# Performance work log

Measured on AMD Instinct MI355X. Metric: run time of the kernel, lower is better.

## Reference

```python
import jax, jax.numpy as jnp
import numpy as np

M, LAM, MAX_ITER, TOL, BETA = 5, 1e-4, 50, 0.01, 1.0


def anderson_fixed_point(lin_w, lin_b, x0):
    """Anderson acceleration for x = Linear(x), faithful to the torch loop.
    x0: (bsz, d, H, W); the fixed-point map applies the linear over W."""
    bsz = x0.shape[0]
    n = x0.size // bsz
    shape = x0.shape
    dt = x0.dtype

    def f(v_flat):  # (bsz, n) -> (bsz, n)
        return (v_flat.reshape(shape) @ lin_w.T + lin_b).reshape(bsz, n)

    x0f = x0.reshape(bsz, n)
    F0 = f(x0f)
    X = jnp.zeros((bsz, M, n), dt).at[:, 0].set(x0f).at[:, 1].set(F0)
    Fm = jnp.zeros((bsz, M, n), dt).at[:, 0].set(F0).at[:, 1].set(f(F0))
    y = jnp.zeros((bsz, M + 1), dt).at[:, 0].set(1.0)
    eyeM = jnp.eye(M, dtype=dt)

    def cond(c):
        _, _, k, res = c
        return (k < MAX_ITER) & (res >= TOL)

    def body(c):
        X, Fm, k, _ = c
        nk = jnp.minimum(k, M)
        # mask inactive history slots (k < M early iterations); padded rows/cols
        # get lam on the diagonal and 0 border -> alpha_j = 0 there, identical
        # to torch's solve on the leading (n+1)x(n+1) submatrix.
        mask = (jnp.arange(M) < nk).astype(dt)               # (M,)
        G = (Fm - X) * mask[None, :, None]                   # (bsz, M, n)
        Hin = jnp.einsum('bin,bjn->bij', G, G) + LAM * eyeM  # (bsz, M, M)
        H = jnp.zeros((bsz, M + 1, M + 1), dt)
        H = H.at[:, 0, 1:].set(mask).at[:, 1:, 0].set(mask).at[:, 1:, 1:].set(Hin)
        alpha = jnp.linalg.solve(H, y[..., None])[:, 1:, 0]  # (bsz, M)
        xnew = BETA * jnp.einsum('bm,bmn->bn', alpha, Fm) + (1.0 - BETA) * jnp.einsum('bm,bmn->bn', alpha, X)
        idx = k % M
        X = X.at[:, idx].set(xnew)
        fnew = f(xnew)
        Fm = Fm.at[:, idx].set(fnew)
        res = jnp.linalg.norm(fnew - xnew) / (1e-5 + jnp.linalg.norm(fnew))
        return (X, Fm, k + 1, res)

    Xf, _, kf, _ = jax.lax.while_loop(
        cond, body, (X, Fm, jnp.int32(2), jnp.asarray(jnp.inf, dt)))
    return Xf[:, (kf - 1) % M].reshape(shape)


def setup_inputs() -> dict:
    key = jax.random.key(0)
    k1, k2, k3, k4, k5 = jax.random.split(key, 5)
    B, D, H, W = 16, 8, 128, 512  # in_features = out_features = W = 512
    x = jax.random.normal(k1, (B, D, H, W), jnp.float32)
    # contractive inner linear so the fixed-point iteration behaves
    lin_w = jax.random.normal(k2, (W, W), jnp.float32) * 0.02
    lin_b = jax.random.normal(k3, (W,), jnp.float32) * 0.1
    weight = jax.random.normal(k4, (W, W), jnp.float32) * 0.02
    bias = jax.random.normal(k5, (W,), jnp.float32) * 0.1
    return {"x": x, "lin_w": lin_w, "lin_b": lin_b, "weight": weight, "bias": bias}


def reference(x, lin_w, lin_b, weight, bias):
    # torch runs the solver under no_grad -> stop_gradient for fidelity
    x_star = anderson_fixed_point(
        jax.lax.stop_gradient(lin_w),
        jax.lax.stop_gradient(lin_b),
        jax.lax.stop_gradient(x))
    return x_star @ weight.T + bias
```

## Files before the change

### kernel.cpp

```cpp
#include <hip/hip_runtime.h>
#include <math.h>

#define FD     512
#define NBATCH 16
#define NROWS  16384
#define ROWS   64
#define NBLK   (NROWS/ROWS)
#define TPB    1024
#define MM     5
#define LAMV   1e-4f
#define MAXIT  50
#define TOLV   0.01f
#define NTOT   8388608
#define PADW   520

typedef __attribute__((ext_vector_type(8))) short  short8;
typedef __attribute__((ext_vector_type(4))) float  float4v;

__device__ unsigned short g_Fm[MM][NTOT];
__device__ unsigned short g_G [MM][NTOT];
__device__ unsigned short g_xb[NTOT];
__device__ unsigned short g_Wb [FD*FD];
__device__ unsigned short g_WbO[FD*FD];
__device__ float g_acc [MAXIT-2][NBATCH][8];
__device__ float g_acc0[NBATCH][8];

static __device__ __forceinline__ unsigned short f2bf(float f) {
    unsigned u = __float_as_uint(f);
    u += 0x7fff + ((u >> 16) & 1);
    return (unsigned short)(u >> 16);
}
static __device__ __forceinline__ float bf2f(unsigned short s) {
    return __uint_as_float(((unsigned)s) << 16);
}

template<int MODE>
static __device__ __forceinline__ void mfma_gemm(const unsigned short* __restrict__ Wb,
                                                 const float* __restrict__ bvec,
                                                 const unsigned short* AsIn,
                                                 unsigned short* FsOut,
                                                 float* __restrict__ gout)
{
    const int lane = threadIdx.x & 63;
    const int wv   = threadIdx.x >> 6;
    const int lm   = lane & 15;
    const int quad = lane >> 4;
    float4v acc[4][2];
#pragma unroll
    for (int ct = 0; ct < 2; ct++) {
        const float b = bvec[wv*32 + ct*16 + lm];
#pragma unroll
        for (int r16 = 0; r16 < 4; r16++) {
            acc[r16][ct][0]=b; acc[r16][ct][1]=b; acc[r16][ct][2]=b; acc[r16][ct][3]=b;
        }
    }
#pragma unroll
    for (int q = 0; q < 4; q++) {
#pragma unroll
        for (int kb = 0; kb < 4; kb++) {
            const int ko = q*128 + kb*32 + quad*8;
            short8 bf[2];
#pragma unroll
            for (int ct = 0; ct < 2; ct++)
                bf[ct] = *(const short8*)(Wb + (wv*32 + ct*16 + lm)*FD + ko);
            short8 af[4];
#pragma unroll
            for (int r16 = 0; r16 < 4; r16++)
                af[r16] = *(const short8*)(AsIn + (r16*16 + lm)*PADW + ko);
#pragma unroll
            for (int r16 = 0; r16 < 4; r16++) {
                acc[r16][0] = __builtin_amdgcn_mfma_f32_16x16x32_bf16(af[r16], bf[0], acc[r16][0], 0,0,0);
                acc[r16][1] = __builtin_amdgcn_mfma_f32_16x16x32_bf16(af[r16], bf[1], acc[r16][1], 0,0,0);
            }
        }
    }
#pragma unroll
    for (int ct = 0; ct < 2; ct++) {
        const int c = wv*32 + ct*16 + lm;
#pragma unroll
        for (int r16 = 0; r16 < 4; r16++)
#pragma unroll
            for (int r = 0; r < 4; r++) {
                const int row = r16*16 + quad*4 + r;
                if (MODE == 0) FsOut[row*PADW + c] = f2bf(acc[r16][ct][r]);
                else           gout[row*FD + c]    = acc[r16][ct][r];
            }
    }
}

static __device__ __forceinline__ void red6(const float vals[6], float (*redS)[8], float* accrow)
{
    const int lane = threadIdx.x & 63, wv = threadIdx.x >> 6;
#pragma unroll
    for (int j = 0; j < 6; j++) {
        float v = vals[j];
#pragma unroll
        for (int o = 32; o; o >>= 1) v += __shfl_down(v, o);
        if (lane == 0) redS[wv][j] = v;
    }
    __syncthreads();
    if (threadIdx.x < 6) {
        float s = 0.f;
#pragma unroll
        for (int w = 0; w < 16; w++) s += redS[w][threadIdx.x];
        atomicAdd(accrow + threadIdx.x, s);
    }
}

__global__ void __launch_bounds__(256) k_init0(const float* __restrict__ lin_w,
                                               const float* __restrict__ weight)
{
    const int i0 = blockIdx.x*256 + threadIdx.x, stride = gridDim.x*256;
    for (int i = i0; i < FD*FD; i += stride) {
        g_Wb [i] = f2bf(lin_w[i]);
        g_WbO[i] = f2bf(weight[i]);
    }
    float* a = &g_acc[0][0][0];
    for (int i = i0; i < (MAXIT-2)*NBATCH*8; i += stride) a[i] = 0.f;
    float* a0 = &g_acc0[0][0];
    for (int i = i0; i < NBATCH*8; i += stride) a0[i] = 0.f;
}

__global__ void __launch_bounds__(TPB, 4) k_init1(const float* __restrict__ x,
                                                  const float* __restrict__ lin_b)
{
    __shared__ __align__(16) unsigned short As[ROWS*PADW];
    __shared__ __align__(16) unsigned short Fs[ROWS*PADW];
    __shared__ float redS[16][8];
    const int tid = threadIdx.x;
    const int t = blockIdx.x, b = t >> 4;
    const int base = t * (ROWS*FD);

#pragma unroll
    for (int i = 0; i < 4; i++) {
        const int e = (i*TPB + tid) * 8;
        const float4 a0 = *(const float4*)(x + base + e);
        const float4 a1 = *(const float4*)(x + base + e + 4);
        short8 v;
        v[0]=f2bf(a0.x); v[1]=f2bf(a0.y); v[2]=f2bf(a0.z); v[3]=f2bf(a0.w);
        v[4]=f2bf(a1.x); v[5]=f2bf(a1.y); v[6]=f2bf(a1.z); v[7]=f2bf(a1.w);
        *(short8*)(As + (e>>9)*PADW + (e&511)) = v;
    }
    __syncthreads();
    mfma_gemm<0>(g_Wb, lin_b, As, Fs, nullptr);
    __syncthreads();
    float d00 = 0.f;
#pragma unroll
    for (int i = 0; i < 4; i++) {
        const int e = (i*TPB + tid) * 8;
        const int off = base + e, lo = (e>>9)*PADW + (e&511);
        const short8 fv = *(const short8*)(Fs + lo);
        const short8 xv = *(const short8*)(As + lo);
        short8 gv;
#pragma unroll
        for (int j = 0; j < 8; j++) {
            const float g = bf2f((unsigned short)fv[j]) - bf2f((unsigned short)xv[j]);
            gv[j] = (short)f2bf(g);
            d00 = fmaf(g, g, d00);
        }
        *(short8*)(&g_Fm[0][off]) = fv;
        *(short8*)(&g_G [0][off]) = gv;
    }
    __syncthreads();
    mfma_gemm<0>(g_Wb, lin_b, Fs, As, nullptr);
    __syncthreads();
    float d01 = 0.f, d11 = 0.f;
#pragma unroll
    for (int i = 0; i < 4; i++) {
        const int e = (i*TPB + tid) * 8;
        const int off = base + e, lo = (e>>9)*PADW + (e&511);
        const short8 f1 = *(const short8*)(As + lo);
        const short8 f0 = *(const short8*)(Fs + lo);
        const short8 g0 = *(const short8*)(&g_G[0][off]);
        short8 gv;
#pragma unroll
        for (int j = 0; j < 8; j++) {
            const float g = bf2f((unsigned short)f1[j]) - bf2f((unsigned short)f0[j]);
            gv[j] = (short)f2bf(g);
            d11 = fmaf(g, g, d11);
            d01 = fmaf(bf2f((unsigned short)g0[j]), g, d01);
        }
        *(short8*)(&g_Fm[1][off]) = f1;
        *(short8*)(&g_G [1][off]) = gv;
    }
    const float vals[6] = {d00, d01, d11, 0.f, 0.f, 0.f};
    red6(vals, redS, &g_acc0[b][0]);
}

__global__ void __launch_bounds__(TPB, 4) k_iter(const float* __restrict__ lin_b, int k)
{
    __shared__ __align__(16) unsigned short As[ROWS*PADW];
    __shared__ __align__(16) unsigned short Fs[ROWS*PADW];
    __shared__ float gramS[MM][MM];
    __shared__ float alphaS[MM];
    __shared__ float Hs[48];
    __shared__ float redS[16][8];
    __shared__ float sres;

    const int tid = threadIdx.x;
    const int t = blockIdx.x, b = t >> 4;
    const int base = t * (ROWS*FD);
    const int it = k - 2, idx = k % MM, nk = (k < MM) ? k : MM;

    if (k > 2) {
        float v = 0.f;
        if (tid < 32) {
            const int bb = tid & 15;
            const int jj = (tid < 16) ? ((k-1) % MM) : 5;
            v = g_acc[it-1][bb][jj];
        }
        v += __shfl_xor(v, 1); v += __shfl_xor(v, 2);
        v += __shfl_xor(v, 4); v += __shfl_xor(v, 8);
        const float num = __shfl(v, 0), den = __shfl(v, 16);
        if (tid == 0) sres = sqrtf(num) / (1e-5f + sqrtf(den));
    }
    __syncthreads();
    if (k > 2 && sres < TOLV) return;

    if (tid == 0) {
#pragma unroll
        for (int i = 0; i < MM; i++)
#pragma unroll
            for (int j = 0; j < MM; j++) gramS[i][j] = 0.f;
        gramS[0][0] = g_acc0[b][0];
        gramS[0][1] = gramS[1][0] = g_acc0[b][1];
        gramS[1][1] = g_acc0[b][2];
        const int j0 = (k - 5 > 2) ? (k - 5) : 2;
        for (int j = j0; j < k; j++) {
            const int ij = j % MM, nkj = (j < MM) ? j : MM;
            for (int c = 0; c < MM; c++)
                if (c < nkj || c == ij) {
                    const float vv = g_acc[j-2][b][c];
                    gramS[ij][c] = vv; gramS[c][ij] = vv;
                }
        }
        float* H = Hs;
        for (int i = 0; i < 42; i++) H[i] = 0.f;
        for (int j = 0; j < nk; j++) { H[1+j] = 1.f; H[(1+j)*7] = 1.f; }
#pragma unroll
        for (int i = 0; i < MM; i++) H[(1+i)*7 + (1+i)] = LAMV;
        for (int i = 0; i < nk; i++)
            for (int j = 0; j < nk; j++)
                H[(1+i)*7 + (1+j)] = gramS[i][j] + (i == j ? LAMV : 0.f);
        H[6] = 1.f;
        for (int col = 0; col < 6; col++) {
            int p = col; float mx = fabsf(H[col*7+col]);
            for (int r2 = col+1; r2 < 6; r2++) {
                const float vv = fabsf(H[r2*7+col]);
                if (vv > mx) { mx = vv; p = r2; }
            }
            if (p != col)
                for (int j = col; j < 7; j++) { const float tt = H[col*7+j]; H[col*7+j] = H[p*7+j]; H[p*7+j] = tt; }
            const float piv = H[col*7+col];
            for (int r2 = col+1; r2 < 6; r2++) {
                const float fct = H[r2*7+col] / piv;
                for (int j = col+1; j < 7; j++) H[r2*7+j] -= fct * H[col*7+j];
            }
        }
        for (int r2 = 5; r2 >= 0; r2--) {
            float s = H[r2*7+6];
            for (int j = r2+1; j < 6; j++) s -= H[r2*7+j] * H[j*7+6];
            H[r2*7+6] = s / H[r2*7+r2];
        }
#pragma unroll
        for (int m = 0; m < MM; m++) alphaS[m] = H[(1+m)*7+6];
    }
    __syncthreads();

    float al[MM];
#pragma unroll
    for (int m = 0; m < MM; m++) al[m] = alphaS[m];

    if (nk == MM) {
#pragma unroll
        for (int i = 0; i < 4; i++) {
            const int e = (i*TPB + tid) * 8;
            const int off = base + e;
            float s[8] = {0,0,0,0,0,0,0,0};
#pragma unroll
            for (int m = 0; m < MM; m++) {
                const short8 fm = *(const short8*)(&g_Fm[m][off]);
#pragma unroll
                for (int j = 0; j < 8; j++)
                    s[j] = fmaf(al[m], bf2f((unsigned short)fm[j]), s[j]);
            }
            short8 v;
#pragma unroll
            for (int j = 0; j < 8; j++) v[j] = (short)f2bf(s[j]);
            *(short8*)(As + (e>>9)*PADW + (e&511)) = v;
            *(short8*)(&g_xb[off]) = v;
        }
    } else {
#pragma unroll
        for (int i = 0; i < 4; i++) {
            const int e = (i*TPB + tid) * 8;
            const int off = base + e;
            float s[8] = {0,0,0,0,0,0,0,0};
            for (int m = 0; m < nk; m++) {
                const short8 fm = *(const short8*)(&g_Fm[m][off]);
#pragma unroll
                for (int j = 0; j < 8; j++)
                    s[j] = fmaf(al[m], bf2f((unsigned short)fm[j]), s[j]);
            }
            short8 v;
#pragma unroll
            for (int j = 0; j < 8; j++) v[j] = (short)f2bf(s[j]);
            *(short8*)(As + (e>>9)*PADW + (e&511)) = v;
            *(short8*)(&g_xb[off]) = v;
        }
    }
    __syncthreads();
    mfma_gemm<0>(g_Wb, lin_b, As, Fs, nullptr);
    __syncthreads();
    float dv[6] = {0,0,0,0,0,0};
    float dself = 0.f;
#pragma unroll
    for (int i = 0; i < 4; i++) {
        const int e = (i*TPB + tid) * 8;
        const int off = base + e, lo = (e>>9)*PADW + (e&511);
        const short8 fv = *(const short8*)(Fs + lo);
        const short8 xv = *(const short8*)(As + lo);
        float gg[8]; short8 gv;
#pragma unroll
        for (int j = 0; j < 8; j++) {
            const float ff = bf2f((unsigned short)fv[j]);
            const float g  = ff - bf2f((unsigned short)xv[j]);
            gg[j] = g; gv[j] = (short)f2bf(g);
            dv[5] = fmaf(ff, ff, dv[5]);
            dself = fmaf(g, g, dself);
        }
        *(short8*)(&g_Fm[idx][off]) = fv;
        *(short8*)(&g_G [idx][off]) = gv;
#pragma unroll
        for (int js = 0; js < MM; js++) {
            if (js != idx && js < nk) {
                const short8 gj = *(const short8*)(&g_G[js][off]);
#pragma unroll
                for (int j = 0; j < 8; j++)
                    dv[js] = fmaf(gg[j], bf2f((unsigned short)gj[j]), dv[js]);
            }
        }
    }
    float vals[6];
#pragma unroll
    for (int j = 0; j < MM; j++) vals[j] = (j == idx) ? (dv[j] + dself) : dv[j];
    vals[5] = dv[5];
    red6(vals, redS, &g_acc[it][b][0]);
}

__global__ void __launch_bounds__(TPB, 4) k_final(const float* __restrict__ bias,
                                                  float* __restrict__ out)
{
    __shared__ __align__(16) unsigned short As[ROWS*PADW];
    const int tid = threadIdx.x;
    const int base = blockIdx.x * (ROWS*FD);
#pragma unroll
    for (int i = 0; i < 4; i++) {
        const int e = (i*TPB + tid) * 8;
        *(short8*)(As + (e>>9)*PADW + (e&511)) = *(const short8*)(&g_xb[base + e]);
    }
    __syncthreads();
    mfma_gemm<1>(g_WbO, bias, As, nullptr, out + base);
}

extern "C" void kernel_launch(void* const* d_in, const int* in_sizes, int n_in,
                              void* d_out, int out_size, void* d_ws, size_t ws_size,
                              hipStream_t stream)
{
    (void)in_sizes; (void)n_in; (void)out_size; (void)d_ws; (void)ws_size;
    const float* x      = (const float*)d_in[0];
    const float* lin_w  = (const float*)d_in[1];
    const float* lin_b  = (const float*)d_in[2];
    const float* weight = (const float*)d_in[3];
    const float* bias   = (const float*)d_in[4];
    float* out = (float*)d_out;

    hipLaunchKernelGGL(k_init0, dim3(512),  dim3(256), 0, stream, lin_w, weight);
    hipLaunchKernelGGL(k_init1, dim3(NBLK), dim3(TPB), 0, stream, x, lin_b);
    for (int k = 2; k < MAXIT; k++)
        hipLaunchKernelGGL(k_iter, dim3(NBLK), dim3(TPB), 0, stream, lin_b, k);
    hipLaunchKernelGGL(k_final, dim3(NBLK), dim3(TPB), 0, stream, bias, out);
}
```

Measured before the change: 630.4 us.

## Fuse Anderson iterations into one persistent cooperative kernel with grid syncs

Replaces the chain of init, per-iteration and final kernel launches with a single cooperative kernel. All 256 blocks stay resident and separate iterations with grid.sync. The current iterate stays in LDS across iterations and feeds the final output GEMM directly, so the bf16 x buffer no longer needs a global round-trip. This removes per-launch overhead and kernel-boundary drains. In exchange it needs full-grid co-residency, at one 1024-thread block per CU with about 133 KB of LDS each, and pays grid-wide barrier costs. If the cooperative launch fails it falls back to the old multi-kernel path.

Result: slower. 1.052 ms (+66.9%).

```diff
diff --git a/kernel.cpp b/kernel.cpp
--- a/kernel.cpp
+++ b/kernel.cpp
@@ -1,5 +1,8 @@
 #include <hip/hip_runtime.h>
+#include <hip/hip_cooperative_groups.h>
 #include <math.h>
+
+namespace cg = cooperative_groups;
 
 #define FD     512
 #define NBATCH 16
@@ -107,6 +110,253 @@
     }
 }
 
+__global__ void __launch_bounds__(TPB, 4) k_anderson(
+    const float* __restrict__ x,     const float* __restrict__ lin_w,
+    const float* __restrict__ lin_b, const float* __restrict__ weight,
+    const float* __restrict__ bias,  float* __restrict__ out)
+{
+    cg::grid_group grid = cg::this_grid();
+
+    __shared__ __align__(16) unsigned short As[ROWS*PADW];
+    __shared__ __align__(16) unsigned short Fs[ROWS*PADW];
+    __shared__ float redS[16][8];
+    __shared__ float gramS[MM][MM];
+    __shared__ float alphaS[MM];
+    __shared__ float Hs[48];
+    __shared__ float gAs[MM][MM];
+    __shared__ float ga0S[3];
+    __shared__ float sres;
+
+    const int tid  = threadIdx.x;
+    const int t    = blockIdx.x, b = t >> 4;
+    const int base = t * (ROWS*FD);
+
+    {
+        const int gi = t*TPB + tid;
+        g_Wb [gi] = f2bf(lin_w[gi]);
+        g_WbO[gi] = f2bf(weight[gi]);
+        if (gi < (MAXIT-2)*NBATCH*8) (&g_acc[0][0][0])[gi] = 0.f;
+        if (gi < NBATCH*8)           (&g_acc0[0][0])[gi]   = 0.f;
+    }
+#pragma unroll
+    for (int i = 0; i < 4; i++) {
+        const int e = (i*TPB + tid) * 8;
+        const float4 a0 = *(const float4*)(x + base + e);
+        const float4 a1 = *(const float4*)(x + base + e + 4);
+        short8 v;
+        v[0]=f2bf(a0.x); v[1]=f2bf(a0.y); v[2]=f2bf(a0.z); v[3]=f2bf(a0.w);
+        v[4]=f2bf(a1.x); v[5]=f2bf(a1.y); v[6]=f2bf(a1.z); v[7]=f2bf(a1.w);
+        *(short8*)(As + (e>>9)*PADW + (e&511)) = v;
+    }
+    grid.sync();
+
+    mfma_gemm<0>(g_Wb, lin_b, As, Fs, nullptr);
+    __syncthreads();
+    float d00 = 0.f;
+#pragma unroll
+    for (int i = 0; i < 4; i++) {
+        const int e = (i*TPB + tid) * 8;
+        const int off = base + e, lo = (e>>9)*PADW + (e&511);
+        const short8 fv = *(const short8*)(Fs + lo);
+        const short8 xv = *(const short8*)(As + lo);
+        short8 gv;
+#pragma unroll
+        for (int j = 0; j < 8; j++) {
+            const float g = bf2f((unsigned short)fv[j]) - bf2f((unsigned short)xv[j]);
+            gv[j] = (short)f2bf(g);
+            d00 = fmaf(g, g, d00);
+        }
+        *(short8*)(&g_Fm[0][off]) = fv;
+        *(short8*)(&g_G [0][off]) = gv;
+    }
+    __syncthreads();
+    mfma_gemm<0>(g_Wb, lin_b, Fs, As, nullptr);
+    __syncthreads();
+    float d01 = 0.f, d11 = 0.f;
+#pragma unroll
+    for (int i = 0; i < 4; i++) {
+        const int e = (i*TPB + tid) * 8;
+        const int off = base + e, lo = (e>>9)*PADW + (e&511);
+        const short8 f1 = *(const short8*)(As + lo);
+        const short8 f0 = *(const short8*)(Fs + lo);
+        const short8 g0 = *(const short8*)(&g_G[0][off]);
+        short8 gv;
+#pragma unroll
+        for (int j = 0; j < 8; j++) {
+            const float g = bf2f((unsigned short)f1[j]) - bf2f((unsigned short)f0[j]);
+            gv[j] = (short)f2bf(g);
+            d11 = fmaf(g, g, d11);
+            d01 = fmaf(bf2f((unsigned short)g0[j]), g, d01);
+        }
+        *(short8*)(&g_Fm[1][off]) = f1;
+        *(short8*)(&g_G [1][off]) = gv;
+    }
+    {
+        const float vals[6] = {d00, d01, d11, 0.f, 0.f, 0.f};
+        red6(vals, redS, &g_acc0[b][0]);
+    }
+    grid.sync();
+
+    for (int k = 2; k < MAXIT; k++) {
+        const int it = k - 2, idx = k % MM, nk = (k < MM) ? k : MM;
+        const int j0 = (k - 5 > 2) ? (k - 5) : 2;
+
+        if (k > 2 && (tid >> 6) == 0) {
+            float v = 0.f;
+            if (tid < 32) {
+                const int bb = tid & 15;
+                const int jj = (tid < 16) ? ((k-1) % MM) : 5;
+                v = g_acc[it-1][bb][jj];
+            }
+            v += __shfl_xor(v, 1); v += __shfl_xor(v, 2);
+            v += __shfl_xor(v, 4); v += __shfl_xor(v, 8);
+            const float num = __shfl(v, 0), den = __shfl(v, 16);
+            if (tid == 0) sres = sqrtf(num) / (1e-5f + sqrtf(den));
+        }
+        if ((tid >> 6) == 1) {
+            const int l = tid & 63;
+            if (l < 25) {
+                const int jj = j0 + l/5;
+                if (jj < k) gAs[l/5][l%5] = g_acc[jj-2][b][l%5];
+            } else if (l < 28) {
+                ga0S[l-25] = g_acc0[b][l-25];
+            }
+        }
+        __syncthreads();
+        if (k > 2 && sres < TOLV) break;
+
+        if (tid == 0) {
+#pragma unroll
+            for (int i = 0; i < MM; i++)
+#pragma unroll
+                for (int j = 0; j < MM; j++) gramS[i][j] = 0.f;
+            gramS[0][0] = ga0S[0];
+            gramS[0][1] = gramS[1][0] = ga0S[1];
+            gramS[1][1] = ga0S[2];
+            for (int j = j0; j < k; j++) {
+                const int ij = j % MM, nkj = (j < MM) ? j : MM;
+                for (int c = 0; c < MM; c++)
+                    if (c < nkj || c == ij) {
+                        const float vv = gAs[j - j0][c];
+                        gramS[ij][c] = vv; gramS[c][ij] = vv;
+                    }
+            }
+            float* H = Hs;
+            for (int i = 0; i < 42; i++) H[i] = 0.f;
+            for (int j = 0; j < nk; j++) { H[1+j] = 1.f; H[(1+j)*7] = 1.f; }
+#pragma unroll
+            for (int i = 0; i < MM; i++) H[(1+i)*7 + (1+i)] = LAMV;
+            for (int i = 0; i < nk; i++)
+                for (int j = 0; j < nk; j++)
+                    H[(1+i)*7 + (1+j)] = gramS[i][j] + (i == j ? LAMV : 0.f);
+            H[6] = 1.f;
+            for (int col = 0; col < 6; col++) {
+                int p = col; float mx = fabsf(H[col*7+col]);
+                for (int r2 = col+1; r2 < 6; r2++) {
+                    const float vv = fabsf(H[r2*7+col]);
+                    if (vv > mx) { mx = vv; p = r2; }
+                }
+                if (p != col)
+                    for (int j = col; j < 7; j++) { const float tt = H[col*7+j]; H[col*7+j] = H[p*7+j]; H[p*7+j] = tt; }
+                const float piv = H[col*7+col];
+                for (int r2 = col+1; r2 < 6; r2++) {
+                    const float fct = H[r2*7+col] / piv;
+                    for (int j = col+1; j < 7; j++) H[r2*7+j] -= fct * H[col*7+j];
+                }
+            }
+            for (int r2 = 5; r2 >= 0; r2--) {
+                float s = H[r2*7+6];
+                for (int j = r2+1; j < 6; j++) s -= H[r2*7+j] * H[j*7+6];
+                H[r2*7+6] = s / H[r2*7+r2];
+            }
+#pragma unroll
+            for (int m = 0; m < MM; m++) alphaS[m] = H[(1+m)*7+6];
+        }
+        __syncthreads();
+
+        float al[MM];
+#pragma unroll
+        for (int m = 0; m < MM; m++) al[m] = alphaS[m];
+
+        if (nk == MM) {
+#pragma unroll
+            for (int i = 0; i < 4; i++) {
+                const int e = (i*TPB + tid) * 8;
+                const int off = base + e;
+                float s[8] = {0,0,0,0,0,0,0,0};
+#pragma unroll
+                for (int m = 0; m < MM; m++) {
+                    const short8 fm = *(const short8*)(&g_Fm[m][off]);
+#pragma unroll
+                    for (int j = 0; j < 8; j++)
+                        s[j] = fmaf(al[m], bf2f((unsigned short)fm[j]), s[j]);
+                }
+                short8 v;
+#pragma unroll
+                for (int j = 0; j < 8; j++) v[j] = (short)f2bf(s[j]);
+                *(short8*)(As + (e>>9)*PADW + (e&511)) = v;
+            }
+        } else {
+#pragma unroll
+            for (int i = 0; i < 4; i++) {
+                const int e = (i*TPB + tid) * 8;
+                const int off = base + e;
+                float s[8] = {0,0,0,0,0,0,0,0};
+                for (int m = 0; m < nk; m++) {
+                    const short8 fm = *(const short8*)(&g_Fm[m][off]);
+#pragma unroll
+                    for (int j = 0; j < 8; j++)
+                        s[j] = fmaf(al[m], bf2f((unsigned short)fm[j]), s[j]);
+                }
+                short8 v;
+#pragma unroll
+                for (int j = 0; j < 8; j++) v[j] = (short)f2bf(s[j]);
+                *(short8*)(As + (e>>9)*PADW + (e&511)) = v;
+            }
+        }
+        __syncthreads();
+        mfma_gemm<0>(g_Wb, lin_b, As, Fs, nullptr);
+        __syncthreads();
+        float dv[6] = {0,0,0,0,0,0};
+        float dself = 0.f;
+#pragma unroll
+        for (int i = 0; i < 4; i++) {
+            const int e = (i*TPB + tid) * 8;
+            const int off = base + e, lo = (e>>9)*PADW + (e&511);
+            const short8 fv = *(const short8*)(Fs + lo);
+            const short8 xv = *(const short8*)(As + lo);
+            float gg[8]; short8 gv;
+#pragma unroll
+            for (int j = 0; j < 8; j++) {
+                const float ff = bf2f((unsigned short)fv[j]);
+                const float g  = ff - bf2f((unsigned short)xv[j]);
+                gg[j] = g; gv[j] = (short)f2bf(g);
+                dv[5] = fmaf(ff, ff, dv[5]);
+                dself = fmaf(g, g, dself);
+            }
+            *(short8*)(&g_Fm[idx][off]) = fv;
+            *(short8*)(&g_G [idx][off]) = gv;
+#pragma unroll
+            for (int js = 0; js < MM; js++) {
+                if (js != idx && js < nk) {
+                    const short8 gj = *(const short8*)(&g_G[js][off]);
+#pragma unroll
+                    for (int j = 0; j < 8; j++)
+                        dv[js] = fmaf(gg[j], bf2f((unsigned short)gj[j]), dv[js]);
+                }
+            }
+        }
+        float vals[6];
+#pragma unroll
+        for (int j = 0; j < MM; j++) vals[j] = (j == idx) ? (dv[j] + dself) : dv[j];
+        vals[5] = dv[5];
+        red6(vals, redS, &g_acc[it][b][0]);
+        grid.sync();
+    }
+
+    mfma_gemm<1>(g_WbO, bias, As, nullptr, out + base);
+}
+
 __global__ void __launch_bounds__(256) k_init0(const float* __restrict__ lin_w,
                                                const float* __restrict__ weight)
 {
@@ -375,9 +625,14 @@
     const float* bias   = (const float*)d_in[4];
     float* out = (float*)d_out;
 
-    hipLaunchKernelGGL(k_init0, dim3(512),  dim3(256), 0, stream, lin_w, weight);
-    hipLaunchKernelGGL(k_init1, dim3(NBLK), dim3(TPB), 0, stream, x, lin_b);
-    for (int k = 2; k < MAXIT; k++)
-        hipLaunchKernelGGL(k_iter, dim3(NBLK), dim3(TPB), 0, stream, lin_b, k);
-    hipLaunchKernelGGL(k_final, dim3(NBLK), dim3(TPB), 0, stream, bias, out);
-}
+    void* args[] = {(void*)&x, (void*)&lin_w, (void*)&lin_b,
+                    (void*)&weight, (void*)&bias, (void*)&out};
+    if (hipLaunchCooperativeKernel(reinterpret_cast<const void*>(&k_anderson),
+                                   dim3(NBLK), dim3(TPB), args, 0, stream) != hipSuccess) {
+        hipLaunchKernelGGL(k_init0, dim3(512),  dim3(256), 0, stream, lin_w, weight);
+        hipLaunchKernelGGL(k_init1, dim3(NBLK), dim3(TPB), 0, stream, x, lin_b);
+        for (int k = 2; k < MAXIT; k++)
+            hipLaunchKernelGGL(k_iter, dim3(NBLK), dim3(TPB), 0, stream, lin_b, k);
+        hipLaunchKernelGGL(k_final, dim3(NBLK), dim3(TPB), 0, stream, bias, out);
+    }
+}
```
